# Kernel optimization log

Hardware: AMD Instinct MI355X
Metric: run time of the kernel (lower is better)

Reference implementation:

```python
import jax, jax.numpy as jnp
import numpy as np

EPS = 1e-5  # torch LayerNorm default


def _ln(x, g, b):
    m = jnp.mean(x, axis=-1, keepdims=True)
    v = jnp.mean((x - m) ** 2, axis=-1, keepdims=True)
    return (x - m) / jnp.sqrt(v + EPS) * g + b


def setup_inputs() -> dict:
    key = jax.random.key(0)
    ks = jax.random.split(key, 16)
    B, C, H, S, FF, BINS = 2048, 20, 256, 64, 512, 128
    f32 = jnp.float32
    def w(k, shape, s=0.02):
        return jax.random.normal(k, shape, f32) * s
    return {
        "bitplanes": jax.random.normal(ks[0], (B, C, 8, 8), f32),
        "conv1_w": w(ks[1], (H, C, 3, 3), 0.05), "conv1_b": jnp.zeros((H,), f32),
        "conv2_w": w(ks[2], (H, H, 3, 3), 0.05), "conv2_b": jnp.zeros((H,), f32),
        "in_proj_w": w(ks[3], (3 * H, H)), "in_proj_b": jnp.zeros((3 * H,), f32),
        "out_proj_w": w(ks[4], (H, H)), "out_proj_b": jnp.zeros((H,), f32),
        "ln1_g": jnp.ones((H,), f32), "ln1_b": jnp.zeros((H,), f32),
        "ff1_w": w(ks[5], (FF, H)), "ff1_b": jnp.zeros((FF,), f32),
        "ff2_w": w(ks[6], (H, FF)), "ff2_b": jnp.zeros((H,), f32),
        "ln2_g": jnp.ones((H,), f32), "ln2_b": jnp.zeros((H,), f32),
        "be1_w": w(ks[7], (H, H * S)), "be1_b": jnp.zeros((H,), f32),
        "be2_w": w(ks[8], (H, H)), "be2_b": jnp.zeros((H,), f32),
        "L1_w": w(ks[9], (H, 3 * H)), "L1_b": jnp.zeros((H,), f32),
        "L2_w": w(ks[10], (H, H)), "L2_b": jnp.zeros((H,), f32),
        "Lln_g": jnp.ones((H,), f32), "Lln_b": jnp.zeros((H,), f32),
        "H1_w": w(ks[11], (H, 2 * H)), "H1_b": jnp.zeros((H,), f32),
        "H2_w": w(ks[12], (H, H)), "H2_b": jnp.zeros((H,), f32),
        "Hln_g": jnp.ones((H,), f32), "Hln_b": jnp.zeros((H,), f32),
        "v1_w": w(ks[13], (H, H)), "v1_b": jnp.zeros((H,), f32),
        "v2_w": w(ks[14], (BINS, H)), "v2_b": jnp.zeros((BINS,), f32),
    }


def reference(bitplanes, conv1_w, conv1_b, conv2_w, conv2_b,
              in_proj_w, in_proj_b, out_proj_w, out_proj_b,
              ln1_g, ln1_b, ff1_w, ff1_b, ff2_w, ff2_b, ln2_g, ln2_b,
              be1_w, be1_b, be2_w, be2_b,
              L1_w, L1_b, L2_w, L2_b, Lln_g, Lln_b,
              H1_w, H1_b, H2_w, H2_b, Hln_g, Hln_b,
              v1_w, v1_b, v2_w, v2_b):
    N, T, Hd, nh = 8, 8, 256, 4
    B = bitplanes.shape[0]
    dn = ('NCHW', 'OIHW', 'NCHW')
    # conv encoder on 8x8 board
    x = jax.nn.relu(jax.lax.conv_general_dilated(bitplanes, conv1_w, (1, 1), 'SAME', dimension_numbers=dn) + conv1_b[None, :, None, None])
    x = jax.nn.relu(jax.lax.conv_general_dilated(x, conv2_w, (1, 1), 'SAME', dimension_numbers=dn) + conv2_b[None, :, None, None])
    x = x.reshape(B, Hd, 64).transpose(0, 2, 1)  # [B, 64, 256]
    # TransformerEncoderLayer (post-norm, eval mode => dropout off)
    qkv = x @ in_proj_w.T + in_proj_b  # [B, 64, 768]
    q, k, v = jnp.split(qkv, 3, axis=-1)
    dh = Hd // nh
    heads = lambda t: t.reshape(B, 64, nh, dh).transpose(0, 2, 1, 3)
    q, k, v = heads(q), heads(k), heads(v)
    scale = 1.0 / float(dh) ** 0.5
    a = jax.nn.softmax(jnp.einsum('bhqd,bhkd->bhqk', q, k) * scale, axis=-1)
    o = jnp.einsum('bhqk,bhkd->bhqd', a, v).transpose(0, 2, 1, 3).reshape(B, 64, Hd)
    o = o @ out_proj_w.T + out_proj_b
    x = _ln(x + o, ln1_g, ln1_b)
    ff = jax.nn.relu(x @ ff1_w.T + ff1_b) @ ff2_w.T + ff2_b
    x = _ln(x + ff, ln2_g, ln2_b)
    xf = x.reshape(B, 64 * Hd)  # [B, 16384]
    be = jax.nn.relu(jax.nn.relu(xf @ be1_w.T + be1_b) @ be2_w.T + be2_b)

    def Lnet(zL, zH):
        h = jax.nn.relu(jnp.concatenate([zL, zH, be], axis=-1) @ L1_w.T + L1_b)
        return _ln(jax.nn.relu(h @ L2_w.T + L2_b), Lln_g, Lln_b)

    def Hnet(zH, zL):
        h = jax.nn.relu(jnp.concatenate([zH, zL], axis=-1) @ H1_w.T + H1_b)
        return _ln(jax.nn.relu(h @ H2_w.T + H2_b), Hln_g, Hln_b)

    z0 = jnp.zeros((B, Hd), x.dtype)

    def step(carry, i):
        zH, zL = carry
        zL = Lnet(zL, zH)
        zH = jnp.where((i + 1) % T == 0, Hnet(zH, zL), zH)  # H update every T steps
        return (zH, zL), None

    (zH, zL), _ = jax.lax.scan(step, (z0, z0), jnp.arange(N * T - 1))
    zL = Lnet(zL, zH)
    zH = Hnet(zH, zL)
    return jax.nn.relu(zH @ v1_w.T + v1_b) @ v2_w.T + v2_b  # [B, 128]
```

## Files before the change

### kernel.cpp

```cpp
#include <hip/hip_runtime.h>
#include <hip/hip_bf16.h>
#include <math.h>

#define DEV __device__ __forceinline__

typedef __attribute__((ext_vector_type(8))) short s16x8;
typedef __attribute__((ext_vector_type(4))) float f32x4;

DEV f32x4 MF(s16x8 a, s16x8 b, f32x4 c) {
    return __builtin_amdgcn_mfma_f32_16x16x32_bf16(a, b, c, 0, 0, 0);
}

DEV void split3(float x, unsigned short& h, unsigned short& m, unsigned short& l) {
    const unsigned u = __float_as_uint(x);
    h = (unsigned short)(u >> 16);
    const float r1 = x - __uint_as_float(u & 0xffff0000u);
    const unsigned u1 = __float_as_uint(r1);
    m = (unsigned short)(u1 >> 16);
    const float r2 = r1 - __uint_as_float(u1 & 0xffff0000u);
    l = (unsigned short)(__float_as_uint(r2) >> 16);
}

DEV void split8store(const float v[8], unsigned short* d) {
    s16x8 vh, vm, vl;
#pragma unroll
    for (int j = 0; j < 8; ++j) {
        unsigned short h, m, l;
        split3(v[j], h, m, l);
        vh[j] = (short)h; vm[j] = (short)m; vl[j] = (short)l;
    }
    *(s16x8*)(d) = vh;
    *(s16x8*)(d + 512) = vm;
    *(s16x8*)(d + 1024) = vl;
}

__global__ void k_tpose(const float* __restrict__ in, float* __restrict__ out, int N, int K) {
    int total = N * K;
    for (int idx = blockIdx.x * blockDim.x + threadIdx.x; idx < total; idx += gridDim.x * blockDim.x) {
        int n = idx / K, k = idx - n * K;
        out[k * N + n] = in[idx];
    }
}

__global__ void k_wpack3(const float* __restrict__ W, unsigned short* __restrict__ WP,
                         int K, int NT, int ldw, int stride, int off) {
    const int idx = blockIdx.x * 256 + threadIdx.x;
    const int total = (K >> 5) * NT * 64;
    if (idx >= total) return;
    const int lane = idx & 63;
    const int nt = (idx >> 6) % NT;
    const int ks = idx / (64 * NT);
    const int col = nt * 16 + (lane & 15);
    const int k0 = ks * 32 + ((lane >> 4) << 3);
    const float* src = W + (size_t)col * ldw + (size_t)k0 * stride + off;
    float v[8];
#pragma unroll
    for (int j = 0; j < 8; ++j) v[j] = src[j * stride];
    split8store(v, WP + (size_t)((ks * NT + nt) * 3) * 512 + lane * 8);
}

__global__ __launch_bounds__(256) void k_conv1(const float* __restrict__ in, const float* __restrict__ w,
                                               const float* __restrict__ bias, float* __restrict__ out) {
    __shared__ __align__(16) float img[20 * 100];
    __shared__ __align__(16) float stg[16 * 260];
    const int b = blockIdx.x;
    const int t = threadIdx.x;
    for (int idx = t; idx < 2000; idx += 256) {
        int c = idx / 100, pp = idx - c * 100;
        int y = pp / 10, x = pp - y * 10;
        float v = 0.f;
        if (y >= 1 && y <= 8 && x >= 1 && x <= 8)
            v = in[((size_t)b * 20 + c) * 64 + (y - 1) * 8 + (x - 1)];
        img[idx] = v;
    }
    __syncthreads();
    const int oc = t;
    float acc[64];
    const float bz = bias[oc];
#pragma unroll
    for (int p = 0; p < 64; ++p) acc[p] = bz;
    const float* wrow = w + oc * 180;
    for (int c = 0; c < 20; ++c) {
#pragma unroll
        for (int k = 0; k < 9; ++k) {
            const int ky = k / 3, kx = k - ky * 3;
            const float wv = wrow[c * 9 + k];
            const int base = c * 100 + ky * 10 + kx;
#pragma unroll
            for (int p = 0; p < 64; ++p)
                acc[p] = fmaf(wv, img[base + p + ((p >> 3) << 1)], acc[p]);
        }
    }
#pragma unroll
    for (int cc = 0; cc < 4; ++cc) {
        __syncthreads();
#pragma unroll
        for (int p = 0; p < 16; ++p) stg[p * 260 + t] = acc[cc * 16 + p];
        __syncthreads();
        for (int idx = t; idx < 4096; idx += 256) {
            const int r = idx >> 8, c = idx & 255;
            out[((size_t)b * 64 + cc * 16 + r) * 256 + c] = fmaxf(stg[r * 260 + c], 0.f);
        }
    }
}

__global__ __launch_bounds__(256) void k_conv2mf(const float* __restrict__ a1,
                                                 const unsigned short* __restrict__ WPC2,
                                                 const float* __restrict__ bias,
                                                 float* __restrict__ xout) {
    __shared__ __align__(16) unsigned short AhS[100 * 132];
    __shared__ __align__(16) unsigned short AmS[100 * 132];
    __shared__ __align__(16) unsigned short AlS[100 * 132];
    const int b = blockIdx.x, t = threadIdx.x;
    const int wv = t >> 6, lane = t & 63;
    f32x4 acc[16];
#pragma unroll
    for (int nt = 0; nt < 16; ++nt) acc[nt] = (f32x4){0.f, 0.f, 0.f, 0.f};
    const int pl = lane & 15;
    const int py = pl >> 3, px = pl & 7;
    const int akoff = (lane >> 4) << 3;
    for (int h = 0; h < 2; ++h) {
        __syncthreads();
        for (int idx = t; idx < 12800; idx += 256) {
            const int pr = idx >> 7, c = idx & 127;
            const int Y = pr / 10, X = pr - Y * 10;
            float v = 0.f;
            if (Y >= 1 && Y <= 8 && X >= 1 && X <= 8)
                v = a1[((size_t)b * 64 + (Y - 1) * 8 + X - 1) * 256 + h * 128 + c];
            unsigned short hh, mm, ll;
            split3(v, hh, mm, ll);
            AhS[pr * 132 + c] = hh;
            AmS[pr * 132 + c] = mm;
            AlS[pr * 132 + c] = ll;
        }
        __syncthreads();
#pragma unroll
        for (int tap = 0; tap < 9; ++tap) {
            const int dy = tap / 3, dx = tap - dy * 3;
            const int prow = (wv * 2 + py + dy) * 10 + px + dx;
            const unsigned short* arh = AhS + prow * 132 + akoff;
            const unsigned short* arm = AmS + prow * 132 + akoff;
            const unsigned short* arl = AlS + prow * 132 + akoff;
#pragma unroll
            for (int ks = 0; ks < 4; ++ks) {
                const s16x8 ah = *(const s16x8*)(arh + ks * 32);
                const s16x8 am = *(const s16x8*)(arm + ks * 32);
                const s16x8 al = *(const s16x8*)(arl + ks * 32);
                const unsigned short* bp = WPC2 + (size_t)(tap * 128 + (h * 4 + ks) * 16) * 1536 + lane * 8;
#pragma unroll
                for (int nt = 0; nt < 16; ++nt) {
                    const unsigned short* bb = bp + nt * 1536;
                    const s16x8 bh = *(const s16x8*)(bb);
                    const s16x8 bm = *(const s16x8*)(bb + 512);
                    const s16x8 bl = *(const s16x8*)(bb + 1024);
                    acc[nt] = MF(ah, bh, acc[nt]);
                    acc[nt] = MF(ah, bm, acc[nt]);
                    acc[nt] = MF(am, bh, acc[nt]);
                    acc[nt] = MF(ah, bl, acc[nt]);
                    acc[nt] = MF(al, bh, acc[nt]);
                    acc[nt] = MF(am, bm, acc[nt]);
                }
            }
        }
    }
    const int prow0 = wv * 16 + ((lane >> 4) << 2);
    const int ccol = lane & 15;
#pragma unroll
    for (int nt = 0; nt < 16; ++nt) {
        const float bz = bias[nt * 16 + ccol];
#pragma unroll
        for (int i = 0; i < 4; ++i)
            xout[((size_t)b * 64 + prow0 + i) * 256 + nt * 16 + ccol] = fmaxf(acc[nt][i] + bz, 0.f);
    }
}

__global__ __launch_bounds__(512) void k_attn(const float* __restrict__ x, const float* __restrict__ wqkvT,
                                              const float* __restrict__ bqkv,
                                              unsigned short* __restrict__ oh, unsigned short* __restrict__ om,
                                              unsigned short* __restrict__ ol) {
    __shared__ __align__(16) float qs[64 * 65];
    __shared__ __align__(16) float ks[64 * 68];
    __shared__ __align__(16) float vs[64 * 68];
    __shared__ float pmax[8 * 64];
    __shared__ float psum[8 * 64];
    const int b = blockIdx.x, h = blockIdx.y;
    const int t = threadIdx.x;
    const int d = t & 63;
    const int pg = t >> 6;
    float aq[8], ak[8], av[8];
#pragma unroll
    for (int j = 0; j < 8; ++j) { aq[j] = 0.f; ak[j] = 0.f; av[j] = 0.f; }
    const float* xrow = x + ((size_t)b * 64 + pg * 8) * 256;
    const int colq = h * 64 + d;
    for (int kk = 0; kk < 256; kk += 4) {
        float wq[4], wk[4], wv[4];
#pragma unroll
        for (int i = 0; i < 4; ++i) {
            const float* wr = wqkvT + (size_t)(kk + i) * 768;
            wq[i] = wr[colq]; wk[i] = wr[256 + colq]; wv[i] = wr[512 + colq];
        }
#pragma unroll
        for (int j = 0; j < 8; ++j) {
            const float4 xv = *(const float4*)(xrow + j * 256 + kk);
            aq[j] = fmaf(xv.x, wq[0], aq[j]); aq[j] = fmaf(xv.y, wq[1], aq[j]);
            aq[j] = fmaf(xv.z, wq[2], aq[j]); aq[j] = fmaf(xv.w, wq[3], aq[j]);
            ak[j] = fmaf(xv.x, wk[0], ak[j]); ak[j] = fmaf(xv.y, wk[1], ak[j]);
            ak[j] = fmaf(xv.z, wk[2], ak[j]); ak[j] = fmaf(xv.w, wk[3], ak[j]);
            av[j] = fmaf(xv.x, wv[0], av[j]); av[j] = fmaf(xv.y, wv[1], av[j]);
            av[j] = fmaf(xv.z, wv[2], av[j]); av[j] = fmaf(xv.w, wv[3], av[j]);
        }
    }
    const float bq = bqkv[colq], bk = bqkv[256 + colq], bv = bqkv[512 + colq];
#pragma unroll
    for (int j = 0; j < 8; ++j) {
        const int p = pg * 8 + j;
        qs[p * 65 + d] = aq[j] + bq;
        ks[p * 68 + d] = ak[j] + bk;
        vs[p * 68 + d] = av[j] + bv;
    }
    __syncthreads();
    const int r = t & 63;
    const int cg = t >> 6;
    float sc[8];
#pragma unroll
    for (int j = 0; j < 8; ++j) sc[j] = 0.f;
    for (int kk = 0; kk < 64; kk += 4) {
        float qv[4];
#pragma unroll
        for (int i = 0; i < 4; ++i) qv[i] = qs[r * 65 + kk + i];
#pragma unroll
        for (int j = 0; j < 8; ++j) {
            const float4 kv = *(const float4*)(ks + (cg * 8 + j) * 68 + kk);
            sc[j] = fmaf(qv[0], kv.x, sc[j]); sc[j] = fmaf(qv[1], kv.y, sc[j]);
            sc[j] = fmaf(qv[2], kv.z, sc[j]); sc[j] = fmaf(qv[3], kv.w, sc[j]);
        }
    }
    float pm = -1e30f;
#pragma unroll
    for (int j = 0; j < 8; ++j) { sc[j] *= 0.125f; pm = fmaxf(pm, sc[j]); }
    pmax[cg * 64 + r] = pm;
    __syncthreads();
    float m = pmax[r];
#pragma unroll
    for (int i = 1; i < 8; ++i) m = fmaxf(m, pmax[i * 64 + r]);
    float pe[8], ps = 0.f;
#pragma unroll
    for (int j = 0; j < 8; ++j) { pe[j] = __expf(sc[j] - m); ps += pe[j]; }
    psum[cg * 64 + r] = ps;
    __syncthreads();
    float den = psum[r];
#pragma unroll
    for (int i = 1; i < 8; ++i) den += psum[i * 64 + r];
    const float rden = 1.f / den;
#pragma unroll
    for (int j = 0; j < 8; ++j) qs[r * 65 + cg * 8 + j] = pe[j] * rden;
    __syncthreads();
    float oa[8];
#pragma unroll
    for (int j = 0; j < 8; ++j) oa[j] = 0.f;
    for (int c = 0; c < 64; ++c) {
        const float pv = qs[r * 65 + c];
        const float4 v0 = *(const float4*)(vs + c * 68 + cg * 8);
        const float4 v1 = *(const float4*)(vs + c * 68 + cg * 8 + 4);
        oa[0] = fmaf(pv, v0.x, oa[0]); oa[1] = fmaf(pv, v0.y, oa[1]);
        oa[2] = fmaf(pv, v0.z, oa[2]); oa[3] = fmaf(pv, v0.w, oa[3]);
        oa[4] = fmaf(pv, v1.x, oa[4]); oa[5] = fmaf(pv, v1.y, oa[5]);
        oa[6] = fmaf(pv, v1.z, oa[6]); oa[7] = fmaf(pv, v1.w, oa[7]);
    }
#pragma unroll
    for (int j = 0; j < 8; ++j) ks[r * 68 + cg * 8 + j] = oa[j];
    __syncthreads();
    for (int idx = t; idx < 4096; idx += 512) {
        const int rr = idx >> 6, dd = idx & 63;
        const float v = ks[rr * 68 + dd];
        unsigned short hh, mm, ll;
        split3(v, hh, mm, ll);
        const size_t o = ((size_t)b * 64 + rr) * 256 + h * 64 + dd;
        oh[o] = hh;
        om[o] = mm;
        ol[o] = ll;
    }
}

__global__ __launch_bounds__(256) void k_gemm_mf(
    const unsigned short* __restrict__ Ah, const unsigned short* __restrict__ Am,
    const unsigned short* __restrict__ Al,
    const unsigned short* __restrict__ WP, const float* __restrict__ bias,
    float* __restrict__ Cf, unsigned short* __restrict__ Ch, unsigned short* __restrict__ Cm,
    unsigned short* __restrict__ Cl,
    int M, int N, int K, int kChunk, int relu) {
    const int t = threadIdx.x;
    const int wv = t >> 6, lane = t & 63;
    const int row0 = blockIdx.x * 64 + wv * 16;
    const int col0 = blockIdx.y * 64;
    const int NT = N >> 4;
    const int k0 = blockIdx.z * kChunk;
    const int nks = kChunk >> 5;
    f32x4 acc[4];
#pragma unroll
    for (int nt = 0; nt < 4; ++nt) acc[nt] = (f32x4){0.f, 0.f, 0.f, 0.f};
    const int arow = row0 + (lane & 15);
    const size_t aoff = (size_t)arow * K + k0 + ((lane >> 4) << 3);
    const unsigned short* aph = Ah + aoff;
    const unsigned short* apm = Am + aoff;
    const unsigned short* apl = Al + aoff;
    const unsigned short* bp = WP + ((size_t)((k0 >> 5) * NT + (col0 >> 4))) * 1536 + lane * 8;
    const size_t bstride = (size_t)NT * 1536;
    for (int ks = 0; ks < nks; ++ks) {
        const s16x8 ah = *(const s16x8*)aph;
        const s16x8 am = *(const s16x8*)apm;
        const s16x8 al = *(const s16x8*)apl;
        aph += 32; apm += 32; apl += 32;
#pragma unroll
        for (int nt = 0; nt < 4; ++nt) {
            const unsigned short* bb = bp + nt * 1536;
            const s16x8 bh = *(const s16x8*)(bb);
            const s16x8 bm = *(const s16x8*)(bb + 512);
            const s16x8 bl = *(const s16x8*)(bb + 1024);
            acc[nt] = MF(ah, bh, acc[nt]);
            acc[nt] = MF(ah, bm, acc[nt]);
            acc[nt] = MF(am, bh, acc[nt]);
            acc[nt] = MF(ah, bl, acc[nt]);
            acc[nt] = MF(al, bh, acc[nt]);
            acc[nt] = MF(am, bm, acc[nt]);
        }
        bp += bstride;
    }
    const int crow = row0 + ((lane >> 4) << 2);
    const int ccol = col0 + (lane & 15);
    float bz[4];
#pragma unroll
    for (int nt = 0; nt < 4; ++nt) bz[nt] = bias ? bias[ccol + nt * 16] : 0.f;
    if (Ch) {
#pragma unroll
        for (int nt = 0; nt < 4; ++nt) {
#pragma unroll
            for (int i = 0; i < 4; ++i) {
                float v = acc[nt][i] + bz[nt];
                if (relu) v = fmaxf(v, 0.f);
                unsigned short hh, mm, ll;
                split3(v, hh, mm, ll);
                const size_t o = (size_t)(crow + i) * N + ccol + nt * 16;
                Ch[o] = hh;
                Cm[o] = mm;
                Cl[o] = ll;
            }
        }
    } else {
        float* base = Cf + (size_t)blockIdx.z * M * N;
#pragma unroll
        for (int nt = 0; nt < 4; ++nt) {
#pragma unroll
            for (int i = 0; i < 4; ++i) {
                float v = acc[nt][i] + bz[nt];
                if (relu) v = fmaxf(v, 0.f);
                base[(size_t)(crow + i) * N + ccol + nt * 16] = v;
            }
        }
    }
}

__global__ __launch_bounds__(256) void k_ln_add(float* __restrict__ x, const float* __restrict__ add,
                                                const float* __restrict__ g, const float* __restrict__ bta,
                                                unsigned short* __restrict__ sh, unsigned short* __restrict__ sm,
                                                unsigned short* __restrict__ sl) {
    const int t = threadIdx.x;
    const size_t r = (size_t)blockIdx.x * 4 + (t >> 6);
    const int lane = t & 63;
    float4 xv = *(const float4*)(x + r * 256 + lane * 4);
    const float4 av = *(const float4*)(add + r * 256 + lane * 4);
    const float4 v = make_float4(xv.x + av.x, xv.y + av.y, xv.z + av.z, xv.w + av.w);
    float s = v.x + v.y + v.z + v.w;
    float ss = fmaf(v.x, v.x, fmaf(v.y, v.y, fmaf(v.z, v.z, v.w * v.w)));
#pragma unroll
    for (int m = 32; m; m >>= 1) { s += __shfl_xor(s, m); ss += __shfl_xor(ss, m); }
    const float mean = s * (1.f / 256.f);
    const float var = ss * (1.f / 256.f) - mean * mean;
    const float rstd = rsqrtf(var + 1e-5f);
    const float4 g4 = *(const float4*)(g + lane * 4);
    const float4 b4 = *(const float4*)(bta + lane * 4);
    float4 ov;
    ov.x = (v.x - mean) * rstd * g4.x + b4.x;
    ov.y = (v.y - mean) * rstd * g4.y + b4.y;
    ov.z = (v.z - mean) * rstd * g4.z + b4.z;
    ov.w = (v.w - mean) * rstd * g4.w + b4.w;
    *(float4*)(x + r * 256 + lane * 4) = ov;
    const float vv[4] = {ov.x, ov.y, ov.z, ov.w};
    unsigned short hh[4], mm[4], ll[4];
#pragma unroll
    for (int j = 0; j < 4; ++j) split3(vv[j], hh[j], mm[j], ll[j]);
    *(ushort4*)(sh + r * 256 + lane * 4) = make_ushort4(hh[0], hh[1], hh[2], hh[3]);
    *(ushort4*)(sm + r * 256 + lane * 4) = make_ushort4(mm[0], mm[1], mm[2], mm[3]);
    *(ushort4*)(sl + r * 256 + lane * 4) = make_ushort4(ll[0], ll[1], ll[2], ll[3]);
}

__global__ void k_be1_reduce(const float* __restrict__ parts, const float* __restrict__ bias,
                             unsigned short* __restrict__ oh, unsigned short* __restrict__ om,
                             unsigned short* __restrict__ ol, int n) {
    const int idx = blockIdx.x * blockDim.x + threadIdx.x;
    if (idx < n) {
        float s = bias[idx & 255];
#pragma unroll
        for (int p = 0; p < 8; ++p) s += parts[(size_t)p * n + idx];
        s = fmaxf(s, 0.f);
        unsigned short hh, mm, ll;
        split3(s, hh, mm, ll);
        oh[idx] = hh;
        om[idx] = mm;
        ol[idx] = ll;
    }
}

DEV void splitpass(const float* scr, unsigned short* frag, int t) {
    const int ks = t >> 6, ln = t & 63;
    const int row = ln & 15;
    const int k0 = ks * 32 + ((ln >> 4) << 3);
    const float* s = scr + row * 260 + k0;
    const float4 p = *(const float4*)s;
    const float4 q = *(const float4*)(s + 4);
    const float v[8] = {p.x, p.y, p.z, p.w, q.x, q.y, q.z, q.w};
    split8store(v, frag + (ks * 3) * 512 + ln * 8);
}

DEV void mfma6(f32x4& acc, s16x8 ah, s16x8 am, s16x8 al, const unsigned short* bp) {
    const s16x8 bh = *(const s16x8*)(bp);
    const s16x8 bm = *(const s16x8*)(bp + 512);
    const s16x8 bl = *(const s16x8*)(bp + 1024);
    acc = MF(ah, bh, acc);
    acc = MF(ah, bm, acc);
    acc = MF(am, bh, acc);
    acc = MF(ah, bl, acc);
    acc = MF(al, bh, acc);
    acc = MF(am, bm, acc);
}

DEV void rungemm(f32x4& a0, f32x4& a1, const unsigned short* __restrict__ WP, int KS,
                 const unsigned short* f0, const unsigned short* f1, const unsigned short* f2,
                 int wv, int lane) {
    for (int ks = 0; ks < KS; ++ks) {
        const unsigned short* fa = (ks < 8) ? f0 : ((ks < 16) ? f1 : f2);
        const int kl = ks & 7;
        const unsigned short* ap = fa + (kl * 3) * 512 + lane * 8;
        const s16x8 ah = *(const s16x8*)(ap);
        const s16x8 am = *(const s16x8*)(ap + 512);
        const s16x8 al = *(const s16x8*)(ap + 1024);
        const unsigned short* bp = WP + (size_t)((ks * 16 + wv * 2) * 3) * 512 + lane * 8;
        mfma6(a0, ah, am, al, bp);
        mfma6(a1, ah, am, al, bp + 1536);
    }
}

DEV void storeC(f32x4 a0, f32x4 a1, const float* __restrict__ bias, float* scr, int wv, int lane) {
    const int rb = (lane >> 4) * 4;
    const int c0 = wv * 32 + (lane & 15);
    const float bz0 = bias[c0];
    const float bz1 = bias[c0 + 16];
    scr[(rb + 0) * 260 + c0] = fmaxf(a0[0] + bz0, 0.f);
    scr[(rb + 1) * 260 + c0] = fmaxf(a0[1] + bz0, 0.f);
    scr[(rb + 2) * 260 + c0] = fmaxf(a0[2] + bz0, 0.f);
    scr[(rb + 3) * 260 + c0] = fmaxf(a0[3] + bz0, 0.f);
    scr[(rb + 0) * 260 + c0 + 16] = fmaxf(a1[0] + bz1, 0.f);
    scr[(rb + 1) * 260 + c0 + 16] = fmaxf(a1[1] + bz1, 0.f);
    scr[(rb + 2) * 260 + c0 + 16] = fmaxf(a1[2] + bz1, 0.f);
    scr[(rb + 3) * 260 + c0 + 16] = fmaxf(a1[3] + bz1, 0.f);
}

DEV void lnpass(float* scr, const float* __restrict__ g, const float* __restrict__ bb, int t) {
    const int row = 2 * (t >> 6) + ((t & 63) >> 5);
    const int c0 = (t & 31) * 8;
    float* s = scr + row * 260 + c0;
    const float4 x0 = *(const float4*)s;
    const float4 x1 = *(const float4*)(s + 4);
    float sum = x0.x + x0.y + x0.z + x0.w + x1.x + x1.y + x1.z + x1.w;
    float sq = fmaf(x0.x, x0.x, fmaf(x0.y, x0.y, fmaf(x0.z, x0.z, x0.w * x0.w)));
    sq = fmaf(x1.x, x1.x, fmaf(x1.y, x1.y, fmaf(x1.z, x1.z, fmaf(x1.w, x1.w, sq))));
#pragma unroll
    for (int m = 16; m; m >>= 1) { sum += __shfl_xor(sum, m); sq += __shfl_xor(sq, m); }
    const float mean = sum * (1.f / 256.f);
    const float var = sq * (1.f / 256.f) - mean * mean;
    const float rstd = rsqrtf(var + 1e-5f);
    const float4 g0 = *(const float4*)(g + c0);
    const float4 g1 = *(const float4*)(g + c0 + 4);
    const float4 b0 = *(const float4*)(bb + c0);
    const float4 b1 = *(const float4*)(bb + c0 + 4);
    float4 o0, o1;
    o0.x = (x0.x - mean) * rstd * g0.x + b0.x;
    o0.y = (x0.y - mean) * rstd * g0.y + b0.y;
    o0.z = (x0.z - mean) * rstd * g0.z + b0.z;
    o0.w = (x0.w - mean) * rstd * g0.w + b0.w;
    o1.x = (x1.x - mean) * rstd * g1.x + b1.x;
    o1.y = (x1.y - mean) * rstd * g1.y + b1.y;
    o1.z = (x1.z - mean) * rstd * g1.z + b1.z;
    o1.w = (x1.w - mean) * rstd * g1.w + b1.w;
    *(float4*)s = o0;
    *(float4*)(s + 4) = o1;
}

__global__ __launch_bounds__(512, 1) void k_hrm(const float* __restrict__ be,
        const unsigned short* __restrict__ L1P, const float* __restrict__ L1b,
        const unsigned short* __restrict__ L2P, const float* __restrict__ L2b,
        const float* __restrict__ Lg, const float* __restrict__ Lbt,
        const unsigned short* __restrict__ H1P, const float* __restrict__ H1b,
        const unsigned short* __restrict__ H2P, const float* __restrict__ H2b,
        const float* __restrict__ Hg, const float* __restrict__ Hbt,
        const unsigned short* __restrict__ v1P, const float* __restrict__ v1b,
        const float* __restrict__ v2T, const float* __restrict__ v2b,
        float* __restrict__ out) {
    __shared__ __align__(16) unsigned short fzL[12288];
    __shared__ __align__(16) unsigned short fzH[12288];
    __shared__ __align__(16) unsigned short fbe[12288];
    __shared__ __align__(16) unsigned short fh1[12288];
    __shared__ __align__(16) float scr[16 * 260];
    const int t = threadIdx.x;
    const int b0 = blockIdx.x * 16;
    const int wv = t >> 6, lane = t & 63;
    for (int i = t; i < 12288; i += 512) { fzL[i] = 0; fzH[i] = 0; }
    {
        const int ks = t >> 6, ln = t & 63;
        const int row = ln & 15;
        const int k0 = ks * 32 + ((ln >> 4) << 3);
        const float* s = be + (size_t)(b0 + row) * 256 + k0;
        const float4 p = *(const float4*)s;
        const float4 q = *(const float4*)(s + 4);
        const float v[8] = {p.x, p.y, p.z, p.w, q.x, q.y, q.z, q.w};
        split8store(v, fbe + (ks * 3) * 512 + ln * 8);
    }
    __syncthreads();
    const f32x4 zero4 = {0.f, 0.f, 0.f, 0.f};
    for (int it = 0; it < 64; ++it) {
        f32x4 a0 = zero4, a1 = zero4;
        rungemm(a0, a1, L1P, 24, fzL, fzH, fbe, wv, lane);
        storeC(a0, a1, L1b, scr, wv, lane);
        __syncthreads();
        splitpass(scr, fh1, t);
        __syncthreads();
        a0 = zero4; a1 = zero4;
        rungemm(a0, a1, L2P, 8, fh1, fh1, fh1, wv, lane);
        storeC(a0, a1, L2b, scr, wv, lane);
        __syncthreads();
        lnpass(scr, Lg, Lbt, t);
        __syncthreads();
        splitpass(scr, fzL, t);
        __syncthreads();
        if (((it + 1) & 7) == 0) {
            a0 = zero4; a1 = zero4;
            rungemm(a0, a1, H1P, 16, fzH, fzL, fzL, wv, lane);
            storeC(a0, a1, H1b, scr, wv, lane);
            __syncthreads();
            splitpass(scr, fh1, t);
            __syncthreads();
            a0 = zero4; a1 = zero4;
            rungemm(a0, a1, H2P, 8, fh1, fh1, fh1, wv, lane);
            storeC(a0, a1, H2b, scr, wv, lane);
            __syncthreads();
            lnpass(scr, Hg, Hbt, t);
            __syncthreads();
            splitpass(scr, fzH, t);
            __syncthreads();
        }
    }
    f32x4 a0 = zero4, a1 = zero4;
    rungemm(a0, a1, v1P, 8, fzH, fzH, fzH, wv, lane);
    storeC(a0, a1, v1b, scr, wv, lane);
    __syncthreads();
    for (int idx = t; idx < 2048; idx += 512) {
        const int r = idx >> 7, oo = idx & 127;
        float s = v2b[oo];
        for (int kk = 0; kk < 256; kk += 4) {
            const float4 c4 = *(const float4*)(&scr[r * 260 + kk]);
            s = fmaf(c4.x, v2T[(kk + 0) * 128 + oo], s);
            s = fmaf(c4.y, v2T[(kk + 1) * 128 + oo], s);
            s = fmaf(c4.z, v2T[(kk + 2) * 128 + oo], s);
            s = fmaf(c4.w, v2T[(kk + 3) * 128 + oo], s);
        }
        out[(size_t)(b0 + r) * 128 + oo] = s;
    }
}

extern "C" void kernel_launch(void* const* d_in, const int* in_sizes, int n_in,
                              void* d_out, int out_size, void* d_ws, size_t ws_size,
                              hipStream_t stream) {
    const float* bitplanes  = (const float*)d_in[0];
    const float* conv1_w    = (const float*)d_in[1];
    const float* conv1_b    = (const float*)d_in[2];
    const float* conv2_w    = (const float*)d_in[3];
    const float* conv2_b    = (const float*)d_in[4];
    const float* in_proj_w  = (const float*)d_in[5];
    const float* in_proj_b  = (const float*)d_in[6];
    const float* out_proj_w = (const float*)d_in[7];
    const float* out_proj_b = (const float*)d_in[8];
    const float* ln1_g      = (const float*)d_in[9];
    const float* ln1_b      = (const float*)d_in[10];
    const float* ff1_w      = (const float*)d_in[11];
    const float* ff1_b      = (const float*)d_in[12];
    const float* ff2_w      = (const float*)d_in[13];
    const float* ff2_b      = (const float*)d_in[14];
    const float* ln2_g      = (const float*)d_in[15];
    const float* ln2_b      = (const float*)d_in[16];
    const float* be1_w      = (const float*)d_in[17];
    const float* be1_b      = (const float*)d_in[18];
    const float* be2_w      = (const float*)d_in[19];
    const float* be2_b      = (const float*)d_in[20];
    const float* L1_w       = (const float*)d_in[21];
    const float* L1_b       = (const float*)d_in[22];
    const float* L2_w       = (const float*)d_in[23];
    const float* L2_b       = (const float*)d_in[24];
    const float* Lln_g      = (const float*)d_in[25];
    const float* Lln_b      = (const float*)d_in[26];
    const float* H1_w       = (const float*)d_in[27];
    const float* H1_b       = (const float*)d_in[28];
    const float* H2_w       = (const float*)d_in[29];
    const float* H2_b       = (const float*)d_in[30];
    const float* Hln_g      = (const float*)d_in[31];
    const float* Hln_b      = (const float*)d_in[32];
    const float* v1_w       = (const float*)d_in[33];
    const float* v1_b       = (const float*)d_in[34];
    const float* v2_w       = (const float*)d_in[35];
    const float* v2_b       = (const float*)d_in[36];

    const size_t persist = 9306112ull;
    int CB = 64;
    for (int c = 2048; c >= 64; c >>= 1) {
        size_t needBytes = ((size_t)c * 106880ull + persist) * 4ull;
        if (needBytes <= ws_size) { CB = c; break; }
    }
    const int NCH = 2048 / CB;

    float* ws = (float*)d_ws;
    float* a1buf = ws;
    float* xbuf  = a1buf + (size_t)CB * 16384;
    float* sbuf  = xbuf + (size_t)CB * 16384;
    float* tbuf  = sbuf + (size_t)CB * 24576;
    float* bemf  = tbuf + (size_t)CB * 49152;
    float* wqkvT = bemf + (size_t)CB * 384;
    float* v2T   = wqkvT + 196608;
    float* L1Pf  = v2T + 32768;
    float* L2Pf  = L1Pf + 294912;
    float* H1Pf  = L2Pf + 98304;
    float* H2Pf  = H1Pf + 196608;
    float* v1Pf  = H2Pf + 98304;
    float* beB   = v1Pf + 98304;
    float* wpOf  = beB + 524288;
    float* wpF1f = wpOf + 98304;
    float* wpF2f = wpF1f + 196608;
    float* wpB1f = wpF2f + 196608;
    float* wpB2f = wpB1f + 6291456;
    float* wpC2f = wpB2f + 98304;

    unsigned short* soh = (unsigned short*)sbuf;
    unsigned short* som = soh + (size_t)CB * 16384;
    unsigned short* sol = som + (size_t)CB * 16384;
    unsigned short* tbh = (unsigned short*)tbuf;
    unsigned short* tbm = tbh + (size_t)CB * 32768;
    unsigned short* tbl = tbm + (size_t)CB * 32768;
    unsigned short* bemh = (unsigned short*)bemf;
    unsigned short* bemm = bemh + (size_t)CB * 256;
    unsigned short* beml = bemm + (size_t)CB * 256;
    unsigned short* L1P = (unsigned short*)L1Pf;
    unsigned short* L2P = (unsigned short*)L2Pf;
    unsigned short* H1P = (unsigned short*)H1Pf;
    unsigned short* H2P = (unsigned short*)H2Pf;
    unsigned short* v1P = (unsigned short*)v1Pf;
    unsigned short* wpO = (unsigned short*)wpOf;
    unsigned short* wpF1 = (unsigned short*)wpF1f;
    unsigned short* wpF2 = (unsigned short*)wpF2f;
    unsigned short* wpB1 = (unsigned short*)wpB1f;
    unsigned short* wpB2 = (unsigned short*)wpB2f;
    unsigned short* wpC2 = (unsigned short*)wpC2f;

    k_tpose<<<256, 256, 0, stream>>>(in_proj_w, wqkvT, 768, 256);
    k_tpose<<<64, 256, 0, stream>>>(v2_w, v2T, 128, 256);
    k_wpack3<<<96, 256, 0, stream>>>(L1_w, L1P, 768, 16, 768, 1, 0);
    k_wpack3<<<32, 256, 0, stream>>>(L2_w, L2P, 256, 16, 256, 1, 0);
    k_wpack3<<<64, 256, 0, stream>>>(H1_w, H1P, 512, 16, 512, 1, 0);
    k_wpack3<<<32, 256, 0, stream>>>(H2_w, H2P, 256, 16, 256, 1, 0);
    k_wpack3<<<32, 256, 0, stream>>>(v1_w, v1P, 256, 16, 256, 1, 0);
    k_wpack3<<<32, 256, 0, stream>>>(out_proj_w, wpO, 256, 16, 256, 1, 0);
    k_wpack3<<<64, 256, 0, stream>>>(ff1_w, wpF1, 256, 32, 256, 1, 0);
    k_wpack3<<<64, 256, 0, stream>>>(ff2_w, wpF2, 512, 16, 512, 1, 0);
    k_wpack3<<<2048, 256, 0, stream>>>(be1_w, wpB1, 16384, 16, 16384, 1, 0);
    k_wpack3<<<32, 256, 0, stream>>>(be2_w, wpB2, 256, 16, 256, 1, 0);
    for (int tap = 0; tap < 9; ++tap)
        k_wpack3<<<32, 256, 0, stream>>>(conv2_w, wpC2 + (size_t)tap * 196608, 256, 16, 2304, 9, tap);

    for (int ch = 0; ch < NCH; ++ch) {
        const float* bp_c = bitplanes + (size_t)ch * CB * 20 * 64;
        k_conv1<<<CB, 256, 0, stream>>>(bp_c, conv1_w, conv1_b, a1buf);
        k_conv2mf<<<CB, 256, 0, stream>>>(a1buf, wpC2, conv2_b, xbuf);
        k_attn<<<dim3(CB, 4), 512, 0, stream>>>(xbuf, wqkvT, in_proj_b, soh, som, sol);
        k_gemm_mf<<<dim3(CB, 4, 1), 256, 0, stream>>>(soh, som, sol, wpO, out_proj_b,
                                                      tbuf, nullptr, nullptr, nullptr,
                                                      CB * 64, 256, 256, 256, 0);
        k_ln_add<<<CB * 16, 256, 0, stream>>>(xbuf, tbuf, ln1_g, ln1_b, soh, som, sol);
        k_gemm_mf<<<dim3(CB, 8, 1), 256, 0, stream>>>(soh, som, sol, wpF1, ff1_b,
                                                      nullptr, tbh, tbm, tbl,
                                                      CB * 64, 512, 256, 256, 1);
        k_gemm_mf<<<dim3(CB, 4, 1), 256, 0, stream>>>(tbh, tbm, tbl, wpF2, ff2_b,
                                                      a1buf, nullptr, nullptr, nullptr,
                                                      CB * 64, 256, 512, 512, 0);
        k_ln_add<<<CB * 16, 256, 0, stream>>>(xbuf, a1buf, ln2_g, ln2_b, soh, som, sol);
        k_gemm_mf<<<dim3(CB / 64, 4, 8), 256, 0, stream>>>(soh, som, sol, wpB1, nullptr,
                                                           tbuf, nullptr, nullptr, nullptr,
                                                           CB, 256, 16384, 2048, 0);
        k_be1_reduce<<<CB, 256, 0, stream>>>(tbuf, be1_b, bemh, bemm, beml, CB * 256);
        k_gemm_mf<<<dim3(CB / 64, 4, 1), 256, 0, stream>>>(bemh, bemm, beml, wpB2, be2_b,
                                                           beB + (size_t)ch * CB * 256, nullptr, nullptr, nullptr,
                                                           CB, 256, 256, 256, 1);
    }

    k_hrm<<<128, 512, 0, stream>>>(beB, L1P, L1_b, L2P, L2_b, Lln_g, Lln_b,
                                   H1P, H1_b, H2P, H2_b, Hln_g, Hln_b,
                                   v1P, v1_b, v2T, v2_b, (float*)d_out);
}
```

Measured before the change: 5.957 ms.

## Move QKV projection from scalar FMA in attention kernel to split-bf16 MFMA GEMM

The QKV input projection used to be computed with scalar fp32 FMAs inside the attention kernel, with each block re-reading weights from global memory. It now runs as a separate split-bf16 MFMA GEMM over packed in_proj weights. The conv2 epilogue additionally emits the hi/mid/lo bf16 split of its output so that GEMM can consume it directly. This adds a QKV round trip through global memory plus an extra launch, and buffers are reassigned (tbuf holds QKV, a1buf holds the out-proj result).

```diff
diff --git a/kernel.cpp b/kernel.cpp
--- a/kernel.cpp
+++ b/kernel.cpp
@@ -107,7 +107,10 @@
 __global__ __launch_bounds__(256) void k_conv2mf(const float* __restrict__ a1,
                                                  const unsigned short* __restrict__ WPC2,
                                                  const float* __restrict__ bias,
-                                                 float* __restrict__ xout) {
+                                                 float* __restrict__ xout,
+                                                 unsigned short* __restrict__ xh,
+                                                 unsigned short* __restrict__ xm,
+                                                 unsigned short* __restrict__ xl) {
     __shared__ __align__(16) unsigned short AhS[100 * 132];
     __shared__ __align__(16) unsigned short AmS[100 * 132];
     __shared__ __align__(16) unsigned short AlS[100 * 132];
@@ -169,15 +172,22 @@
     for (int nt = 0; nt < 16; ++nt) {
         const float bz = bias[nt * 16 + ccol];
 #pragma unroll
-        for (int i = 0; i < 4; ++i)
-            xout[((size_t)b * 64 + prow0 + i) * 256 + nt * 16 + ccol] = fmaxf(acc[nt][i] + bz, 0.f);
-    }
-}
-
-__global__ __launch_bounds__(512) void k_attn(const float* __restrict__ x, const float* __restrict__ wqkvT,
-                                              const float* __restrict__ bqkv,
-                                              unsigned short* __restrict__ oh, unsigned short* __restrict__ om,
-                                              unsigned short* __restrict__ ol) {
+        for (int i = 0; i < 4; ++i) {
+            const float v = fmaxf(acc[nt][i] + bz, 0.f);
+            const size_t o = ((size_t)b * 64 + prow0 + i) * 256 + nt * 16 + ccol;
+            xout[o] = v;
+            unsigned short hh, mm, ll;
+            split3(v, hh, mm, ll);
+            xh[o] = hh;
+            xm[o] = mm;
+            xl[o] = ll;
+        }
+    }
+}
+
+__global__ __launch_bounds__(512) void k_attn2(const float* __restrict__ qkv,
+                                               unsigned short* __restrict__ oh, unsigned short* __restrict__ om,
+                                               unsigned short* __restrict__ ol) {
     __shared__ __align__(16) float qs[64 * 65];
     __shared__ __align__(16) float ks[64 * 68];
     __shared__ __align__(16) float vs[64 * 68];
@@ -185,38 +195,16 @@
     __shared__ float psum[8 * 64];
     const int b = blockIdx.x, h = blockIdx.y;
     const int t = threadIdx.x;
-    const int d = t & 63;
-    const int pg = t >> 6;
-    float aq[8], ak[8], av[8];
-#pragma unroll
-    for (int j = 0; j < 8; ++j) { aq[j] = 0.f; ak[j] = 0.f; av[j] = 0.f; }
-    const float* xrow = x + ((size_t)b * 64 + pg * 8) * 256;
-    const int colq = h * 64 + d;
-    for (int kk = 0; kk < 256; kk += 4) {
-        float wq[4], wk[4], wv[4];
-#pragma unroll
-        for (int i = 0; i < 4; ++i) {
-            const float* wr = wqkvT + (size_t)(kk + i) * 768;
-            wq[i] = wr[colq]; wk[i] = wr[256 + colq]; wv[i] = wr[512 + colq];
-        }
-#pragma unroll
-        for (int j = 0; j < 8; ++j) {
-            const float4 xv = *(const float4*)(xrow + j * 256 + kk);
-            aq[j] = fmaf(xv.x, wq[0], aq[j]); aq[j] = fmaf(xv.y, wq[1], aq[j]);
-            aq[j] = fmaf(xv.z, wq[2], aq[j]); aq[j] = fmaf(xv.w, wq[3], aq[j]);
-            ak[j] = fmaf(xv.x, wk[0], ak[j]); ak[j] = fmaf(xv.y, wk[1], ak[j]);
-            ak[j] = fmaf(xv.z, wk[2], ak[j]); ak[j] = fmaf(xv.w, wk[3], ak[j]);
-            av[j] = fmaf(xv.x, wv[0], av[j]); av[j] = fmaf(xv.y, wv[1], av[j]);
-            av[j] = fmaf(xv.z, wv[2], av[j]); av[j] = fmaf(xv.w, wv[3], av[j]);
-        }
-    }
-    const float bq = bqkv[colq], bk = bqkv[256 + colq], bv = bqkv[512 + colq];
-#pragma unroll
-    for (int j = 0; j < 8; ++j) {
-        const int p = pg * 8 + j;
-        qs[p * 65 + d] = aq[j] + bq;
-        ks[p * 68 + d] = ak[j] + bk;
-        vs[p * 68 + d] = av[j] + bv;
+    for (int idx = t; idx < 1024; idx += 512) {
+        const int rr = idx >> 4, cc = (idx & 15) * 4;
+        const float* src = qkv + ((size_t)b * 64 + rr) * 768 + h * 64 + cc;
+        const float4 q4 = *(const float4*)(src);
+        const float4 k4 = *(const float4*)(src + 256);
+        const float4 v4 = *(const float4*)(src + 512);
+        qs[rr * 65 + cc + 0] = q4.x; qs[rr * 65 + cc + 1] = q4.y;
+        qs[rr * 65 + cc + 2] = q4.z; qs[rr * 65 + cc + 3] = q4.w;
+        *(float4*)(ks + rr * 68 + cc) = k4;
+        *(float4*)(vs + rr * 68 + cc) = v4;
     }
     __syncthreads();
     const int r = t & 63;
@@ -618,7 +606,7 @@
     const float* v2_w       = (const float*)d_in[35];
     const float* v2_b       = (const float*)d_in[36];
 
-    const size_t persist = 9306112ull;
+    const size_t persist = 9404416ull;
     int CB = 64;
     for (int c = 2048; c >= 64; c >>= 1) {
         size_t needBytes = ((size_t)c * 106880ull + persist) * 4ull;
@@ -632,8 +620,8 @@
     float* sbuf  = xbuf + (size_t)CB * 16384;
     float* tbuf  = sbuf + (size_t)CB * 24576;
     float* bemf  = tbuf + (size_t)CB * 49152;
-    float* wqkvT = bemf + (size_t)CB * 384;
-    float* v2T   = wqkvT + 196608;
+    float* wpQf  = bemf + (size_t)CB * 384;
+    float* v2T   = wpQf + 294912;
     float* L1Pf  = v2T + 32768;
     float* L2Pf  = L1Pf + 294912;
     float* H1Pf  = L2Pf + 98304;
@@ -656,6 +644,7 @@
     unsigned short* bemh = (unsigned short*)bemf;
     unsigned short* bemm = bemh + (size_t)CB * 256;
     unsigned short* beml = bemm + (size_t)CB * 256;
+    unsigned short* wpQ = (unsigned short*)wpQf;
     unsigned short* L1P = (unsigned short*)L1Pf;
     unsigned short* L2P = (unsigned short*)L2Pf;
     unsigned short* H1P = (unsigned short*)H1Pf;
@@ -668,8 +657,8 @@
     unsigned short* wpB2 = (unsigned short*)wpB2f;
     unsigned short* wpC2 = (unsigned short*)wpC2f;
 
-    k_tpose<<<256, 256, 0, stream>>>(in_proj_w, wqkvT, 768, 256);
     k_tpose<<<64, 256, 0, stream>>>(v2_w, v2T, 128, 256);
+    k_wpack3<<<96, 256, 0, stream>>>(in_proj_w, wpQ, 256, 48, 256, 1, 0);
     k_wpack3<<<96, 256, 0, stream>>>(L1_w, L1P, 768, 16, 768, 1, 0);
     k_wpack3<<<32, 256, 0, stream>>>(L2_w, L2P, 256, 16, 256, 1, 0);
     k_wpack3<<<64, 256, 0, stream>>>(H1_w, H1P, 512, 16, 512, 1, 0);
@@ -686,12 +675,15 @@
     for (int ch = 0; ch < NCH; ++ch) {
         const float* bp_c = bitplanes + (size_t)ch * CB * 20 * 64;
         k_conv1<<<CB, 256, 0, stream>>>(bp_c, conv1_w, conv1_b, a1buf);
-        k_conv2mf<<<CB, 256, 0, stream>>>(a1buf, wpC2, conv2_b, xbuf);
-        k_attn<<<dim3(CB, 4), 512, 0, stream>>>(xbuf, wqkvT, in_proj_b, soh, som, sol);
+        k_conv2mf<<<CB, 256, 0, stream>>>(a1buf, wpC2, conv2_b, xbuf, soh, som, sol);
+        k_gemm_mf<<<dim3(CB, 12, 1), 256, 0, stream>>>(soh, som, sol, wpQ, in_proj_b,
+                                                       tbuf, nullptr, nullptr, nullptr,
+                                                       CB * 64, 768, 256, 256, 0);
+        k_attn2<<<dim3(CB, 4), 512, 0, stream>>>(tbuf, soh, som, sol);
         k_gemm_mf<<<dim3(CB, 4, 1), 256, 0, stream>>>(soh, som, sol, wpO, out_proj_b,
-                                                      tbuf, nullptr, nullptr, nullptr,
+                                                      a1buf, nullptr, nullptr, nullptr,
                                                       CB * 64, 256, 256, 256, 0);
-        k_ln_add<<<CB * 16, 256, 0, stream>>>(xbuf, tbuf, ln1_g, ln1_b, soh, som, sol);
+        k_ln_add<<<CB * 16, 256, 0, stream>>>(xbuf, a1buf, ln1_g, ln1_b, soh, som, sol);
         k_gemm_mf<<<dim3(CB, 8, 1), 256, 0, stream>>>(soh, som, sol, wpF1, ff1_b,
                                                       nullptr, tbh, tbm, tbl,
                                                       CB * 64, 512, 256, 256, 1);
```

Measured after the change: 5.361 ms. 10.0% less time.
